# Performance work log

Measured on AMD Instinct MI355X. Metric: run time of the kernel, lower is better.

Reference implementation:

```python
import jax, jax.numpy as jnp
import numpy as np

B, E, H, W, P, C = 2, 256, 192, 192, 16, 80
GRIDS = (40, 36, 24, 16, 12)
L = len(GRIDS)
MASK_W, CLS_W, ALPHA, GAMMA, EPS = 3.0, 1.0, 0.25, 2.0, 1e-4


def setup_inputs() -> dict:
    key = jax.random.key(0)
    ks = jax.random.split(key, 32)
    inp = {"mask_out": jax.random.normal(ks[0], (B, E, H, W), jnp.float32)}
    for i, g in enumerate(GRIDS):
        inp[f"kernel_l{i}"] = jax.random.normal(ks[1 + i], (B, g, g, E), jnp.float32) * 0.05
        inp[f"cate_l{i}"] = jax.random.uniform(ks[6 + i], (B, g, g, C), jnp.float32)
        inp[f"pos_l{i}"] = jax.random.randint(ks[11 + i], (B, P), 0, g * g, dtype=jnp.int32)
        inp[f"cate_t_l{i}"] = jax.random.randint(ks[16 + i], (B, g, g), -1, C, dtype=jnp.int32)
    # binary instance masks, image-major layout [B, L, P, H, W]
    inp["mask_targets"] = (jax.random.uniform(ks[21], (B, L, P, H, W)) > 0.9).astype(jnp.float32)
    return inp


def _forward(mask_out, kernels, cates, mask_targets, pos_idxs, cate_ts):
    # --- dynamic 1x1 conv: gather positive kernels and apply as batched matmul ---
    preds = []
    for kl, pl in zip(kernels, pos_idxs):
        g2 = kl.shape[1] * kl.shape[2]
        kflat = kl.reshape(B, g2, E)
        kp = jnp.take_along_axis(kflat, pl[:, :, None], axis=1)  # [B, P, E]
        preds.append(jnp.einsum('bpe,behw->bphw', kp, mask_out))  # F.conv2d 1x1
    preds = jnp.stack(preds)  # [L, B, P, H, W]  (level-major, matches torch cat order)

    # --- dice loss ---
    mp = jax.nn.sigmoid(preds).reshape(L * B * P, H * W)
    # NOTE: original code concatenates targets image-major (img, level) while preds
    # are level-major (level, img); we reproduce that pairing faithfully.
    mt = mask_targets.reshape(B * L * P, H * W)
    a = jnp.sum(mp * mt, axis=1)
    b = jnp.sum(mp * mp, axis=1)
    c = jnp.sum(mt * mt, axis=1)
    mask_loss = jnp.sum(1.0 - 2.0 * a / (b + c + 1e-4)) / (L * B * P)

    # --- focal loss on positive grid cells ---
    tgt = jnp.concatenate([t.reshape(-1) for t in cate_ts])            # [N]
    prd = jnp.concatenate([cl.reshape(-1, C) for cl in cates])          # [N, C]
    posm = (tgt > -1).astype(jnp.float32)
    p = jnp.clip(prd, EPS, 1.0 - EPS)
    gt = jax.nn.one_hot(jnp.clip(tgt, 0, C - 1), C, dtype=jnp.float32)
    af = jnp.where(gt == 1.0, ALPHA, 1.0 - ALPHA)
    pt = jnp.where(gt == 1.0, p, 1.0 - p)
    fw = af * (1.0 - pt) ** GAMMA
    ce = -(gt * jnp.log(p) + (1.0 - gt) * jnp.log(1.0 - p))
    cls_loss = jnp.sum(fw * ce * posm[:, None]) / jnp.sum(posm)

    return jnp.stack([MASK_W * mask_loss, CLS_W * cls_loss])  # [mask_loss, cls_loss]


def reference(mask_out, kernel_l0, kernel_l1, kernel_l2, kernel_l3, kernel_l4,
              cate_l0, cate_l1, cate_l2, cate_l3, cate_l4, mask_targets,
              pos_l0, pos_l1, pos_l2, pos_l3, pos_l4,
              cate_t_l0, cate_t_l1, cate_t_l2, cate_t_l3, cate_t_l4):
    return _forward(mask_out,
                    (kernel_l0, kernel_l1, kernel_l2, kernel_l3, kernel_l4),
                    (cate_l0, cate_l1, cate_l2, cate_l3, cate_l4),
                    mask_targets,
                    (pos_l0, pos_l1, pos_l2, pos_l3, pos_l4),
                    (cate_t_l0, cate_t_l1, cate_t_l2, cate_t_l3, cate_t_l4))
```

## Files before the change

### kernel.cpp

```cpp
#include <hip/hip_runtime.h>
#include <hip/hip_bf16.h>

namespace {

constexpr int kHW = 36864;
constexpr int kGemmBlocks = 1152;
constexpr int kFocalBlocks = 605;

typedef __attribute__((ext_vector_type(8))) short bf16x8;
typedef __attribute__((ext_vector_type(4))) float f32x4;

__device__ __forceinline__ unsigned short f2bf(float x) {
  return __builtin_bit_cast(unsigned short, __float2bfloat16(x));
}

__device__ __forceinline__ float wave_sum(float v) {
#pragma unroll
  for (int off = 32; off; off >>= 1) v += __shfl_xor(v, off, 64);
  return v;
}

__global__ __launch_bounds__(256) void prep_kernel(
    const float* __restrict__ k0, const float* __restrict__ k1,
    const float* __restrict__ k2, const float* __restrict__ k3,
    const float* __restrict__ k4,
    const int* __restrict__ q0, const int* __restrict__ q1,
    const int* __restrict__ q2, const int* __restrict__ q3,
    const int* __restrict__ q4,
    unsigned short* __restrict__ kbf, float* __restrict__ acc) {
  const int bid = blockIdx.x;
  if (bid == 0) {
    for (int i = threadIdx.x; i < 482; i += 256) acc[i] = 0.f;
    return;
  }
  const int idx = bid - 1;
  const int b = idx / 80;
  const int row = idx - b * 80;
  if (threadIdx.x >= 128) return;
  const int l = row >> 4, p = row & 15;
  const float* kb[5] = {k0, k1, k2, k3, k4};
  const int* pb[5] = {q0, q1, q2, q3, q4};
  const int bg2[5] = {b * 1600, b * 1296, b * 576, b * 256, b * 144};
  const int pos = pb[l][b * 16 + p];
  const int ch = threadIdx.x * 2;
  const float2 kv = *(const float2*)(kb[l] + (size_t)(bg2[l] + pos) * 256 + ch);
  *(unsigned int*)&kbf[((size_t)b * 80 + row) * 256 + ch] =
      (unsigned int)f2bf(kv.x) | ((unsigned int)f2bf(kv.y) << 16);
}

__global__ __launch_bounds__(256, 2) void mega_kernel(
    const float* __restrict__ mask_out,
    const unsigned short* __restrict__ kbf,
    const float* __restrict__ mask_targets,
    const float* __restrict__ c0, const float* __restrict__ c1,
    const float* __restrict__ c2, const float* __restrict__ c3,
    const float* __restrict__ c4,
    const int* __restrict__ t0, const int* __restrict__ t1,
    const int* __restrict__ t2, const int* __restrict__ t3,
    const int* __restrict__ t4,
    float* __restrict__ acc) {
  __shared__ float bufB[2][64][64];
  __shared__ float bred[4][240];

  const int bid = blockIdx.x;

  if (bid >= kGemmBlocks) {
    const int idx = (bid - kGemmBlocks) * 256 + threadIdx.x;
    const int n = idx / 20;
    const int cq = (idx - n * 20) * 4;
    int t;
    const float* crow;
    if (n < 3200) {
      t = t0[n]; crow = c0 + (size_t)n * 80;
    } else if (n < 5792) {
      const int o = n - 3200; t = t1[o]; crow = c1 + (size_t)o * 80;
    } else if (n < 6944) {
      const int o = n - 5792; t = t2[o]; crow = c2 + (size_t)o * 80;
    } else if (n < 7456) {
      const int o = n - 6944; t = t3[o]; crow = c3 + (size_t)o * 80;
    } else {
      const int o = n - 7456; t = t4[o]; crow = c4 + (size_t)o * 80;
    }
    float term = 0.f, np = 0.f;
    if (t > -1) {
      const float4 pv4 = *(const float4*)&crow[cq];
      const float pvs[4] = {pv4.x, pv4.y, pv4.z, pv4.w};
#pragma unroll
      for (int j = 0; j < 4; ++j) {
        float pv = fminf(fmaxf(pvs[j], 1e-4f), 1.f - 1e-4f);
        const bool gm = (cq + j == t);
        const float af = gm ? 0.25f : 0.75f;
        const float pt = gm ? pv : 1.f - pv;
        const float om = 1.f - pt;
        term = fmaf(af * om * om, -__logf(pt), term);
      }
      if (cq == 0) np = 1.f;
    }
    term = wave_sum(term);
    np = wave_sum(np);
    const int wid = threadIdx.x >> 6;
    if ((threadIdx.x & 63) == 0) {
      bred[0][wid] = term;
      bred[0][4 + wid] = np;
    }
    __syncthreads();
    if (threadIdx.x == 0) {
      unsafeAtomicAdd(&acc[480],
                      bred[0][0] + bred[0][1] + bred[0][2] + bred[0][3]);
      unsafeAtomicAdd(&acc[481],
                      bred[0][4] + bred[0][5] + bred[0][6] + bred[0][7]);
    }
    return;
  }

  const int b = bid / 576;
  const int tile = bid - b * 576;
  const int px0 = tile * 64;
  const int lane = threadIdx.x & 63;
  const int wv = threadIdx.x >> 6;
  const int px16 = lane & 15;
  const int hi8 = (lane >> 4) * 8;
  const int pxl = px0 + wv * 16 + px16;

  const unsigned short* __restrict__ ka =
      kbf + ((size_t)b * 80 + px16) * 256 + hi8;

  const float* __restrict__ gstage = mask_out + (size_t)b * 256 * kHW +
                                     (size_t)(wv * 4 + (lane >> 4)) * kHW +
                                     px0 + (lane & 15) * 4;

#define STAGE(CUR, T)                                                        \
  {                                                                          \
    _Pragma("unroll") for (int r = 0; r < 4; ++r) {                          \
      const float* gs = gstage + (size_t)((T)*64 + r * 16) * kHW;            \
      __builtin_amdgcn_global_load_lds(                                      \
          (const __attribute__((address_space(1))) unsigned int*)gs,         \
          (__attribute__((address_space(3))) unsigned int*)                  \
              &bufB[CUR][r * 16 + wv * 4][0],                                \
          16, 0, 0);                                                         \
    }                                                                        \
  }

  f32x4 a5[5];
#pragma unroll
  for (int mt = 0; mt < 5; ++mt) a5[mt] = (f32x4){0.f, 0.f, 0.f, 0.f};

  STAGE(0, 0);
  __syncthreads();

#pragma unroll
  for (int t = 0; t < 4; ++t) {
    if (t + 1 < 4) STAGE((t + 1) & 1, t + 1);
#pragma unroll
    for (int sub = 0; sub < 2; ++sub) {
      const int ks = t * 2 + sub;
      float fb[8];
#pragma unroll
      for (int j = 0; j < 8; ++j)
        fb[j] = bufB[t & 1][sub * 32 + hi8 + j][wv * 16 + px16];
      bf16x8 bb;
#pragma unroll
      for (int j = 0; j < 8; ++j) bb[j] = (short)f2bf(fb[j]);
#pragma unroll
      for (int mt = 0; mt < 5; ++mt) {
        const bf16x8 af = *(const bf16x8*)(ka + mt * 4096 + ks * 32);
        a5[mt] =
            __builtin_amdgcn_mfma_f32_16x16x32_bf16(af, bb, a5[mt], 0, 0, 0);
      }
    }
    __syncthreads();
  }
#undef STAGE

#pragma unroll
  for (int mt = 0; mt < 5; ++mt) {
#pragma unroll
    for (int j = 0; j < 4; ++j) {
      const int row80 = mt * 16 + (lane >> 4) * 4 + j;
      const int r = (row80 >> 4) * 32 + b * 16 + (row80 & 15);
      const float x0 = a5[mt][j];
      const float mp = 1.f / (1.f + __expf(-x0));
      const float tv = mask_targets[(size_t)r * kHW + pxl];
      float av = mp * tv;
      float bv = mp * mp;
      float cv = tv;
#pragma unroll
      for (int m = 1; m <= 8; m <<= 1) {
        av += __shfl_xor(av, m, 64);
        bv += __shfl_xor(bv, m, 64);
        cv += __shfl_xor(cv, m, 64);
      }
      if (px16 == 0) {
        bred[wv][row80] = av;
        bred[wv][80 + row80] = bv;
        bred[wv][160 + row80] = cv;
      }
    }
  }
  __syncthreads();
  if (threadIdx.x < 240) {
    const int q = threadIdx.x / 80;
    const int row80 = threadIdx.x - q * 80;
    const int r = (row80 >> 4) * 32 + b * 16 + (row80 & 15);
    const float s = bred[0][threadIdx.x] + bred[1][threadIdx.x] +
                    bred[2][threadIdx.x] + bred[3][threadIdx.x];
    unsafeAtomicAdd(&acc[q * 160 + r], s);
  }
}

__global__ __launch_bounds__(64) void finalize_kernel(
    const float* __restrict__ acc, float* __restrict__ out) {
  const int tid = threadIdx.x;
  float s = 0.f;
#pragma unroll
  for (int rr = 0; rr < 3; ++rr) {
    const int r = tid + rr * 64;
    if (r < 160) {
      const float a = acc[r];
      const float bb = acc[160 + r];
      const float cc = acc[320 + r];
      s += 1.f - 2.f * a / (bb + cc + 1e-4f);
    }
  }
  s = wave_sum(s);
  if (tid == 0) {
    out[0] = 3.0f * (s / 160.f);
    out[1] = acc[480] / acc[481];
  }
}

}

extern "C" void kernel_launch(void* const* d_in, const int* in_sizes, int n_in,
                              void* d_out, int out_size, void* d_ws,
                              size_t ws_size, hipStream_t stream) {
  const float* mask_out = (const float*)d_in[0];
  const float* k[5];
  const float* cc[5];
  const int* pp[5];
  const int* tt[5];
  for (int i = 0; i < 5; ++i) {
    k[i] = (const float*)d_in[1 + 4 * i];
    cc[i] = (const float*)d_in[2 + 4 * i];
    pp[i] = (const int*)d_in[3 + 4 * i];
    tt[i] = (const int*)d_in[4 + 4 * i];
  }
  const float* mt = (const float*)d_in[21];
  float* acc = (float*)d_ws;
  unsigned short* kbf = (unsigned short*)((float*)d_ws + 512);
  float* out = (float*)d_out;

  hipLaunchKernelGGL(prep_kernel, dim3(161), dim3(256), 0, stream, k[0], k[1],
                     k[2], k[3], k[4], pp[0], pp[1], pp[2], pp[3], pp[4], kbf,
                     acc);
  hipLaunchKernelGGL(mega_kernel, dim3(kGemmBlocks + kFocalBlocks), dim3(256),
                     0, stream, mask_out, kbf, mt, cc[0], cc[1], cc[2], cc[3],
                     cc[4], tt[0], tt[1], tt[2], tt[3], tt[4], acc);
  hipLaunchKernelGGL(finalize_kernel, dim3(1), dim3(64), 0, stream, acc, out);
}
```

Baseline: 70.03 us.

## Pre-repack mask_out into bf16 MFMA fragment layout in a separate pass

Adds a repack pass, merged into the prep kernel, that converts mask_out from fp32 to bf16. It stores the result in workspace in the exact per-lane B-fragment order the MFMA needs. The GEMM kernel then loads its eight B fragments with direct vector loads, dropping the LDS double-buffer, the per-element conversion and the barriers, and its occupancy hint rises to 4. The cost is an extra global round trip: roughly 38 MB of bf16 written and read back, on top of the original fp32 read. It also adds a kernel-boundary serialization between the repack and the GEMM.

```diff
diff --git a/kernel.cpp b/kernel.cpp
--- a/kernel.cpp
+++ b/kernel.cpp
@@ -4,6 +4,7 @@
 namespace {
 
 constexpr int kHW = 36864;
+constexpr int kRepackBlocks = 2304;
 constexpr int kGemmBlocks = 1152;
 constexpr int kFocalBlocks = 605;
 
@@ -20,36 +21,79 @@
   return v;
 }
 
-__global__ __launch_bounds__(256) void prep_kernel(
+__global__ __launch_bounds__(256, 4) void repack_prep_kernel(
+    const float* __restrict__ mask_out,
     const float* __restrict__ k0, const float* __restrict__ k1,
     const float* __restrict__ k2, const float* __restrict__ k3,
     const float* __restrict__ k4,
     const int* __restrict__ q0, const int* __restrict__ q1,
     const int* __restrict__ q2, const int* __restrict__ q3,
     const int* __restrict__ q4,
-    unsigned short* __restrict__ kbf, float* __restrict__ acc) {
+    unsigned short* __restrict__ moT, unsigned short* __restrict__ kbf,
+    float* __restrict__ acc) {
   const int bid = blockIdx.x;
-  if (bid == 0) {
-    for (int i = threadIdx.x; i < 482; i += 256) acc[i] = 0.f;
+  if (bid >= kRepackBlocks) {
+    const int pid = bid - kRepackBlocks;
+    if (pid == 0) {
+      for (int i = threadIdx.x; i < 482; i += 256) acc[i] = 0.f;
+      return;
+    }
+    const int idx = pid - 1;
+    const int b = idx / 80;
+    const int row = idx - b * 80;
+    if (threadIdx.x >= 128) return;
+    const int l = row >> 4, p = row & 15;
+    const float* kb[5] = {k0, k1, k2, k3, k4};
+    const int* pb[5] = {q0, q1, q2, q3, q4};
+    const int bg2[5] = {b * 1600, b * 1296, b * 576, b * 256, b * 144};
+    const int pos = pb[l][b * 16 + p];
+    const int ch = threadIdx.x * 2;
+    const float2 kv =
+        *(const float2*)(kb[l] + (size_t)(bg2[l] + pos) * 256 + ch);
+    *(unsigned int*)&kbf[((size_t)b * 80 + row) * 256 + ch] =
+        (unsigned int)f2bf(kv.x) | ((unsigned int)f2bf(kv.y) << 16);
     return;
   }
-  const int idx = bid - 1;
-  const int b = idx / 80;
-  const int row = idx - b * 80;
-  if (threadIdx.x >= 128) return;
-  const int l = row >> 4, p = row & 15;
-  const float* kb[5] = {k0, k1, k2, k3, k4};
-  const int* pb[5] = {q0, q1, q2, q3, q4};
-  const int bg2[5] = {b * 1600, b * 1296, b * 576, b * 256, b * 144};
-  const int pos = pb[l][b * 16 + p];
-  const int ch = threadIdx.x * 2;
-  const float2 kv = *(const float2*)(kb[l] + (size_t)(bg2[l] + pos) * 256 + ch);
-  *(unsigned int*)&kbf[((size_t)b * 80 + row) * 256 + ch] =
-      (unsigned int)f2bf(kv.x) | ((unsigned int)f2bf(kv.y) << 16);
-}
-
-__global__ __launch_bounds__(256, 2) void mega_kernel(
-    const float* __restrict__ mask_out,
+
+  const int b = bid / 1152;
+  const int rem = bid - b * 1152;
+  const int ks = rem / 144;
+  const int pxt = rem - ks * 144;
+  const int lane = threadIdx.x & 63;
+  const int wv = threadIdx.x >> 6;
+
+  __shared__ unsigned short ldsC[32][524];
+
+  const float* __restrict__ src =
+      mask_out + (size_t)b * 256 * kHW + (size_t)ks * 32 * kHW + pxt * 256;
+
+#pragma unroll
+  for (int i = 0; i < 8; ++i) {
+    const int ch = wv * 8 + i;
+    const float4 v = *(const float4*)&src[(size_t)ch * kHW + lane * 4];
+    uint2 pk;
+    pk.x = (unsigned int)f2bf(v.x) | ((unsigned int)f2bf(v.y) << 16);
+    pk.y = (unsigned int)f2bf(v.z) | ((unsigned int)f2bf(v.w) << 16);
+    *(uint2*)&ldsC[ch][lane * 4] = pk;
+  }
+  __syncthreads();
+
+  const int px16 = lane & 15, kh = lane >> 4;
+  unsigned short* __restrict__ dstbase =
+      moT + (((size_t)b * 2304 + pxt * 16) * 8 + ks) * 512 + (size_t)lane * 8;
+#pragma unroll
+  for (int f = 0; f < 4; ++f) {
+    const int pxblk = (threadIdx.x >> 6) * 4 + f;
+    const int px = pxblk * 16 + px16;
+    bf16x8 frag;
+#pragma unroll
+    for (int j = 0; j < 8; ++j) frag[j] = (short)ldsC[kh * 8 + j][px];
+    *(bf16x8*)(dstbase + (size_t)pxblk * 4096) = frag;
+  }
+}
+
+__global__ __launch_bounds__(256, 4) void gemm_focal_kernel(
+    const unsigned short* __restrict__ moT,
     const unsigned short* __restrict__ kbf,
     const float* __restrict__ mask_targets,
     const float* __restrict__ c0, const float* __restrict__ c1,
@@ -59,9 +103,7 @@
     const int* __restrict__ t2, const int* __restrict__ t3,
     const int* __restrict__ t4,
     float* __restrict__ acc) {
-  __shared__ float bufB[2][64][64];
   __shared__ float bred[4][240];
-
   const int bid = blockIdx.x;
 
   if (bid >= kGemmBlocks) {
@@ -115,62 +157,36 @@
 
   const int b = bid / 576;
   const int tile = bid - b * 576;
-  const int px0 = tile * 64;
   const int lane = threadIdx.x & 63;
   const int wv = threadIdx.x >> 6;
   const int px16 = lane & 15;
   const int hi8 = (lane >> 4) * 8;
-  const int pxl = px0 + wv * 16 + px16;
+  const int pxblk = tile * 4 + wv;
+  const int pxl = pxblk * 16 + px16;
+
+  const unsigned short* __restrict__ bsrc =
+      moT + ((size_t)(b * 2304 + pxblk) * 8) * 512 + (size_t)lane * 8;
+  bf16x8 bfr[8];
+#pragma unroll
+  for (int ks = 0; ks < 8; ++ks)
+    bfr[ks] = *(const bf16x8*)(bsrc + (size_t)ks * 512);
 
   const unsigned short* __restrict__ ka =
       kbf + ((size_t)b * 80 + px16) * 256 + hi8;
 
-  const float* __restrict__ gstage = mask_out + (size_t)b * 256 * kHW +
-                                     (size_t)(wv * 4 + (lane >> 4)) * kHW +
-                                     px0 + (lane & 15) * 4;
-
-#define STAGE(CUR, T)                                                        \
-  {                                                                          \
-    _Pragma("unroll") for (int r = 0; r < 4; ++r) {                          \
-      const float* gs = gstage + (size_t)((T)*64 + r * 16) * kHW;            \
-      __builtin_amdgcn_global_load_lds(                                      \
-          (const __attribute__((address_space(1))) unsigned int*)gs,         \
-          (__attribute__((address_space(3))) unsigned int*)                  \
-              &bufB[CUR][r * 16 + wv * 4][0],                                \
-          16, 0, 0);                                                         \
-    }                                                                        \
-  }
-
   f32x4 a5[5];
 #pragma unroll
   for (int mt = 0; mt < 5; ++mt) a5[mt] = (f32x4){0.f, 0.f, 0.f, 0.f};
 
-  STAGE(0, 0);
-  __syncthreads();
-
-#pragma unroll
-  for (int t = 0; t < 4; ++t) {
-    if (t + 1 < 4) STAGE((t + 1) & 1, t + 1);
-#pragma unroll
-    for (int sub = 0; sub < 2; ++sub) {
-      const int ks = t * 2 + sub;
-      float fb[8];
-#pragma unroll
-      for (int j = 0; j < 8; ++j)
-        fb[j] = bufB[t & 1][sub * 32 + hi8 + j][wv * 16 + px16];
-      bf16x8 bb;
-#pragma unroll
-      for (int j = 0; j < 8; ++j) bb[j] = (short)f2bf(fb[j]);
-#pragma unroll
-      for (int mt = 0; mt < 5; ++mt) {
-        const bf16x8 af = *(const bf16x8*)(ka + mt * 4096 + ks * 32);
-        a5[mt] =
-            __builtin_amdgcn_mfma_f32_16x16x32_bf16(af, bb, a5[mt], 0, 0, 0);
-      }
-    }
-    __syncthreads();
-  }
-#undef STAGE
+#pragma unroll
+  for (int ks = 0; ks < 8; ++ks) {
+#pragma unroll
+    for (int mt = 0; mt < 5; ++mt) {
+      const bf16x8 af = *(const bf16x8*)(ka + mt * 4096 + ks * 32);
+      a5[mt] =
+          __builtin_amdgcn_mfma_f32_16x16x32_bf16(af, bfr[ks], a5[mt], 0, 0, 0);
+    }
+  }
 
 #pragma unroll
   for (int mt = 0; mt < 5; ++mt) {
@@ -178,8 +194,7 @@
     for (int j = 0; j < 4; ++j) {
       const int row80 = mt * 16 + (lane >> 4) * 4 + j;
       const int r = (row80 >> 4) * 32 + b * 16 + (row80 & 15);
-      const float x0 = a5[mt][j];
-      const float mp = 1.f / (1.f + __expf(-x0));
+      const float mp = 1.f / (1.f + __expf(-a5[mt][j]));
       const float tv = mask_targets[(size_t)r * kHW + pxl];
       float av = mp * tv;
       float bv = mp * mp;
@@ -246,15 +261,18 @@
     tt[i] = (const int*)d_in[4 + 4 * i];
   }
   const float* mt = (const float*)d_in[21];
-  float* acc = (float*)d_ws;
-  unsigned short* kbf = (unsigned short*)((float*)d_ws + 512);
+
+  char* ws = (char*)d_ws;
+  float* acc = (float*)ws;
+  unsigned short* kbf = (unsigned short*)(ws + 4096);
+  unsigned short* moT = (unsigned short*)(ws + 90112);
   float* out = (float*)d_out;
 
-  hipLaunchKernelGGL(prep_kernel, dim3(161), dim3(256), 0, stream, k[0], k[1],
-                     k[2], k[3], k[4], pp[0], pp[1], pp[2], pp[3], pp[4], kbf,
-                     acc);
-  hipLaunchKernelGGL(mega_kernel, dim3(kGemmBlocks + kFocalBlocks), dim3(256),
-                     0, stream, mask_out, kbf, mt, cc[0], cc[1], cc[2], cc[3],
-                     cc[4], tt[0], tt[1], tt[2], tt[3], tt[4], acc);
+  hipLaunchKernelGGL(repack_prep_kernel, dim3(kRepackBlocks + 161), dim3(256),
+                     0, stream, mask_out, k[0], k[1], k[2], k[3], k[4], pp[0],
+                     pp[1], pp[2], pp[3], pp[4], moT, kbf, acc);
+  hipLaunchKernelGGL(gemm_focal_kernel, dim3(kGemmBlocks + kFocalBlocks),
+                     dim3(256), 0, stream, moT, kbf, mt, cc[0], cc[1], cc[2],
+                     cc[3], cc[4], tt[0], tt[1], tt[2], tt[3], tt[4], acc);
   hipLaunchKernelGGL(finalize_kernel, dim3(1), dim3(64), 0, stream, acc, out);
 }
```

New measurement: 74.32 us. 6.1% more time.
